# Performance work log

Hardware: AMD Instinct MI355X
Metric: run time of the kernel (lower is better)

Reference implementation:

```python
import jax, jax.numpy as jnp
import numpy as np

B, S, D, H = 2, 2048, 1024, 16
HD = D // H
EPS = 1e-5


def setup_inputs() -> dict:
    key = jax.random.key(0)
    ks = jax.random.split(key, 10)
    s = 1.0 / np.sqrt(D)
    return {
        "x": jax.random.normal(ks[0], (B, S, D), jnp.float32),
        "wq": jax.random.normal(ks[1], (D, D), jnp.float32) * s,
        "bq": jnp.zeros((D,), jnp.float32),
        "wk": jax.random.normal(ks[2], (D, D), jnp.float32) * s,
        "bk": jnp.zeros((D,), jnp.float32),
        "wv": jax.random.normal(ks[3], (D, D), jnp.float32) * s,
        "bv": jnp.zeros((D,), jnp.float32),
        "wo": jax.random.normal(ks[4], (D, D), jnp.float32) * s,
        "bo": jnp.zeros((D,), jnp.float32),
        "gamma": jnp.ones((D,), jnp.float32),
        "beta": jnp.zeros((D,), jnp.float32),
    }


def reference(x, wq, bq, wk, bk, wv, bv, wo, bo, gamma, beta):
    b, s, d = x.shape
    # QKV projections (torch Linear: y = x @ W^T + b)
    q = (x @ wq.T + bq).reshape(b, s, H, HD)
    k = (x @ wk.T + bk).reshape(b, s, H, HD)
    v = (x @ wv.T + bv).reshape(b, s, H, HD)
    # scores: [b, h, s, s], scaled by sqrt(d_model) as in the source
    scores = jnp.einsum("bqhd,bkhd->bhqk", q, k) / np.sqrt(D)
    attn = jax.nn.softmax(scores, axis=-1)
    ctx = jnp.einsum("bhqk,bkhd->bqhd", attn, v).reshape(b, s, d)
    # output projection (dropout is identity in eval mode)
    residual = ctx @ wo.T + bo
    y = x + residual
    # LayerNorm over last dim
    mu = jnp.mean(y, axis=-1, keepdims=True)
    var = jnp.var(y, axis=-1, keepdims=True)
    return (y - mu) / jnp.sqrt(var + EPS) * gamma + beta
```

## Files before the change

### kernel.cpp

```cpp
#include <hip/hip_runtime.h>
#include <math.h>

#define BBATCH 2
#define SS 2048
#define DMODEL 1024
#define NH 16
#define HD 64
#define MM 4096
#define LNEPS 1e-5f
#define CEXP 0.045084220029831766f

typedef __bf16 bf16_t;
typedef __bf16 bf16x4 __attribute__((ext_vector_type(4)));
typedef __bf16 bf16x8 __attribute__((ext_vector_type(8)));
typedef float f32x4 __attribute__((ext_vector_type(4)));

#define MFMA(a, b, c) __builtin_amdgcn_mfma_f32_16x16x32_bf16(a, b, c, 0, 0, 0)

__device__ __forceinline__ void load_lds16(const bf16_t* g, bf16_t* l) {
    __builtin_amdgcn_global_load_lds(
        (const __attribute__((address_space(1))) void*)g,
        (__attribute__((address_space(3))) void*)l, 16, 0, 0);
}

__global__ __launch_bounds__(256) void cvt_kernel(const float* __restrict__ in,
                                                  bf16_t* __restrict__ out) {
    const int i = (blockIdx.x * 256 + threadIdx.x) * 4;
    float4 f = *(const float4*)(in + i);
    bf16x4 o = {(bf16_t)f.x, (bf16_t)f.y, (bf16_t)f.z, (bf16_t)f.w};
    *(bf16x4*)(out + i) = o;
}

__global__ __launch_bounds__(256, 2) void gemm_qkv(
    const bf16_t* __restrict__ A,
    const bf16_t* __restrict__ Wq, const bf16_t* __restrict__ Wk,
    const bf16_t* __restrict__ Wv,
    const float* __restrict__ bq, const float* __restrict__ bk,
    const float* __restrict__ bv,
    bf16_t* __restrict__ qo, bf16_t* __restrict__ ko, bf16_t* __restrict__ vo)
{
    __shared__ bf16_t As[128 * 32];
    __shared__ bf16_t Bs[128 * 32];
    const int tid = threadIdx.x, L = tid & 63, w = tid >> 6;
    const int quad = L >> 4, l15 = L & 15;
    const int wm = (w >> 1) * 64, wn = (w & 1) * 64;
    const int m0 = blockIdx.x * 128;
    const int mat = blockIdx.y >> 3;
    const int n0 = (blockIdx.y & 7) * 128;
    const bf16_t* W = (mat == 0) ? Wq : ((mat == 1) ? Wk : Wv);

    f32x4 acc[4][4] = {};
    for (int k0 = 0; k0 < DMODEL; k0 += 32) {
        __syncthreads();
        #pragma unroll
        for (int i = 0; i < 2; ++i) {
            const int r = w * 32 + i * 16;
            load_lds16(A + (size_t)(m0 + r + (L >> 2)) * DMODEL + k0 + (L & 3) * 8, &As[r * 32]);
            load_lds16(W + (size_t)(n0 + r + (L >> 2)) * DMODEL + k0 + (L & 3) * 8, &Bs[r * 32]);
        }
        __syncthreads();
        bf16x8 af[4], bfr[4];
        #pragma unroll
        for (int t = 0; t < 4; ++t) af[t] = *(const bf16x8*)&As[(wm + t * 16 + l15) * 32 + quad * 8];
        #pragma unroll
        for (int t = 0; t < 4; ++t) bfr[t] = *(const bf16x8*)&Bs[(wn + t * 16 + l15) * 32 + quad * 8];
        #pragma unroll
        for (int mt = 0; mt < 4; ++mt)
            #pragma unroll
            for (int nt = 0; nt < 4; ++nt)
                acc[mt][nt] = MFMA(af[mt], bfr[nt], acc[mt][nt]);
    }

    if (mat < 2) {
        bf16_t* out = (mat == 0) ? qo : ko;
        const float* bias = (mat == 0) ? bq : bk;
        const float sc = (mat == 0) ? CEXP : 1.0f;
        #pragma unroll
        for (int nt = 0; nt < 4; ++nt) {
            const int gn = n0 + wn + nt * 16 + l15;
            const int h = gn >> 6, hd = gn & 63;
            const float bb = bias[gn];
            #pragma unroll
            for (int mt = 0; mt < 4; ++mt)
                #pragma unroll
                for (int r = 0; r < 4; ++r) {
                    const int gm = m0 + wm + mt * 16 + quad * 4 + r;
                    const int b = gm >> 11, s = gm & 2047;
                    out[((size_t)((b * NH + h) * SS + s)) * HD + hd] =
                        (bf16_t)((acc[mt][nt][r] + bb) * sc);
                }
        }
    } else {
        #pragma unroll
        for (int nt = 0; nt < 4; ++nt) {
            const int gn = n0 + wn + nt * 16 + l15;
            const int h = gn >> 6, hd = gn & 63;
            const float bb = bv[gn];
            #pragma unroll
            for (int mt = 0; mt < 4; ++mt) {
                const int gm0 = m0 + wm + mt * 16 + quad * 4;
                const int b = gm0 >> 11, s0 = gm0 & 2047;
                bf16x4 o = {(bf16_t)(acc[mt][nt][0] + bb), (bf16_t)(acc[mt][nt][1] + bb),
                            (bf16_t)(acc[mt][nt][2] + bb), (bf16_t)(acc[mt][nt][3] + bb)};
                *(bf16x4*)(vo + ((size_t)((b * NH + h) * HD + hd)) * SS + s0) = o;
            }
        }
    }
}

__global__ __launch_bounds__(256, 2) void gemm_out(
    const bf16_t* __restrict__ A, const bf16_t* __restrict__ W,
    const float* __restrict__ bias, const float* __restrict__ resid,
    float* __restrict__ out)
{
    __shared__ bf16_t As[128 * 32];
    __shared__ bf16_t Bs[128 * 32];
    const int tid = threadIdx.x, L = tid & 63, w = tid >> 6;
    const int quad = L >> 4, l15 = L & 15;
    const int wm = (w >> 1) * 64, wn = (w & 1) * 64;
    const int m0 = blockIdx.x * 128;
    const int n0 = blockIdx.y * 128;

    f32x4 acc[4][4] = {};
    for (int k0 = 0; k0 < DMODEL; k0 += 32) {
        __syncthreads();
        #pragma unroll
        for (int i = 0; i < 2; ++i) {
            const int r = w * 32 + i * 16;
            load_lds16(A + (size_t)(m0 + r + (L >> 2)) * DMODEL + k0 + (L & 3) * 8, &As[r * 32]);
            load_lds16(W + (size_t)(n0 + r + (L >> 2)) * DMODEL + k0 + (L & 3) * 8, &Bs[r * 32]);
        }
        __syncthreads();
        bf16x8 af[4], bfr[4];
        #pragma unroll
        for (int t = 0; t < 4; ++t) af[t] = *(const bf16x8*)&As[(wm + t * 16 + l15) * 32 + quad * 8];
        #pragma unroll
        for (int t = 0; t < 4; ++t) bfr[t] = *(const bf16x8*)&Bs[(wn + t * 16 + l15) * 32 + quad * 8];
        #pragma unroll
        for (int mt = 0; mt < 4; ++mt)
            #pragma unroll
            for (int nt = 0; nt < 4; ++nt)
                acc[mt][nt] = MFMA(af[mt], bfr[nt], acc[mt][nt]);
    }
    #pragma unroll
    for (int nt = 0; nt < 4; ++nt) {
        const int gn = n0 + wn + nt * 16 + l15;
        const float bb = bias[gn];
        #pragma unroll
        for (int mt = 0; mt < 4; ++mt)
            #pragma unroll
            for (int r = 0; r < 4; ++r) {
                const int gm = m0 + wm + mt * 16 + quad * 4 + r;
                const size_t idx = (size_t)gm * DMODEL + gn;
                out[idx] = acc[mt][nt][r] + bb + resid[idx];
            }
    }
}

__global__ __launch_bounds__(256, 2) void flash_kernel(
    const bf16_t* __restrict__ Q, const bf16_t* __restrict__ K,
    const bf16_t* __restrict__ VT, bf16_t* __restrict__ ctx)
{
    __shared__ bf16_t Kt[64 * 64];
    __shared__ bf16_t Vt[64 * 64];
    const int tid = threadIdx.x, L = tid & 63, w = tid >> 6;
    const int quad = L >> 4, l15 = L & 15, l7 = L & 7;
    const int bh = blockIdx.y, b = bh >> 4, h = bh & 15;
    const int q0 = blockIdx.x * 128;
    const bf16_t* Qb = Q + (size_t)bh * SS * HD;
    const bf16_t* Kb = K + (size_t)bh * SS * HD;
    const bf16_t* Vb = VT + (size_t)bh * HD * SS;

    bf16x8 qf[2][2];
    #pragma unroll
    for (int g = 0; g < 2; ++g) {
        const int qrow = q0 + (w * 2 + g) * 16 + l15;
        #pragma unroll
        for (int c = 0; c < 2; ++c)
            qf[g][c] = *(const bf16x8*)(Qb + (size_t)qrow * HD + c * 32 + quad * 8);
    }

    f32x4 accO[2][4] = {};
    float l_s[2] = {0.f, 0.f};

    const int srow = L >> 3;
    const int schk = ((l7 ^ srow)) * 8;

    for (int kt = 0; kt < SS / 64; ++kt) {
        __syncthreads();
        #pragma unroll
        for (int i = 0; i < 2; ++i) {
            const int r0 = w * 16 + i * 8;
            load_lds16(Kb + (size_t)(kt * 64 + r0 + srow) * HD + schk, &Kt[r0 * 64]);
            load_lds16(Vb + (size_t)(r0 + srow) * SS + kt * 64 + schk, &Vt[r0 * 64]);
        }
        __syncthreads();

        bf16x8 kf[4][2];
        #pragma unroll
        for (int jt = 0; jt < 4; ++jt)
            #pragma unroll
            for (int c = 0; c < 2; ++c)
                kf[jt][c] = *(const bf16x8*)&Kt[(jt * 16 + l15) * 64 + ((c * 4 + quad) ^ l7) * 8];

        bf16x8 vf[4][2];
        #pragma unroll
        for (int mt = 0; mt < 4; ++mt)
            #pragma unroll
            for (int c = 0; c < 2; ++c) {
                const int base = (mt * 16 + l15) * 64;
                const int ch0 = c * 4 + (quad >> 1);
                bf16x4 lo = *(const bf16x4*)&Vt[base + ((ch0 ^ l7) * 8) + (quad & 1) * 4];
                bf16x4 hi = *(const bf16x4*)&Vt[base + (((ch0 + 2) ^ l7) * 8) + (quad & 1) * 4];
                vf[mt][c] = __builtin_shufflevector(lo, hi, 0, 1, 2, 3, 4, 5, 6, 7);
            }

        #pragma unroll
        for (int g = 0; g < 2; ++g) {
            f32x4 st[4];
            #pragma unroll
            for (int jt = 0; jt < 4; ++jt) {
                f32x4 z = {0.f, 0.f, 0.f, 0.f};
                z = MFMA(kf[jt][0], qf[g][0], z);
                z = MFMA(kf[jt][1], qf[g][1], z);
                st[jt] = z;
            }
            #pragma unroll
            for (int jt = 0; jt < 4; ++jt)
                #pragma unroll
                for (int r = 0; r < 4; ++r)
                    st[jt][r] = exp2f(st[jt][r]);
            float s01 = (st[0][0] + st[0][1]) + (st[0][2] + st[0][3]);
            float s23 = (st[1][0] + st[1][1]) + (st[1][2] + st[1][3]);
            float s45 = (st[2][0] + st[2][1]) + (st[2][2] + st[2][3]);
            float s67 = (st[3][0] + st[3][1]) + (st[3][2] + st[3][3]);
            l_s[g] += (s01 + s23) + (s45 + s67);

            bf16x8 pf0, pf1;
            pf0[0] = (bf16_t)st[0][0]; pf0[1] = (bf16_t)st[0][1];
            pf0[2] = (bf16_t)st[0][2]; pf0[3] = (bf16_t)st[0][3];
            pf0[4] = (bf16_t)st[1][0]; pf0[5] = (bf16_t)st[1][1];
            pf0[6] = (bf16_t)st[1][2]; pf0[7] = (bf16_t)st[1][3];
            pf1[0] = (bf16_t)st[2][0]; pf1[1] = (bf16_t)st[2][1];
            pf1[2] = (bf16_t)st[2][2]; pf1[3] = (bf16_t)st[2][3];
            pf1[4] = (bf16_t)st[3][0]; pf1[5] = (bf16_t)st[3][1];
            pf1[6] = (bf16_t)st[3][2]; pf1[7] = (bf16_t)st[3][3];

            #pragma unroll
            for (int mt = 0; mt < 4; ++mt) {
                accO[g][mt] = MFMA(vf[mt][0], pf0, accO[g][mt]);
                accO[g][mt] = MFMA(vf[mt][1], pf1, accO[g][mt]);
            }
        }
    }

    #pragma unroll
    for (int g = 0; g < 2; ++g) {
        float lsum = l_s[g];
        lsum += __shfl_xor(lsum, 16);
        lsum += __shfl_xor(lsum, 32);
        const float inv = 1.0f / lsum;
        const int s = q0 + (w * 2 + g) * 16 + l15;
        #pragma unroll
        for (int mt = 0; mt < 4; ++mt) {
            bf16x4 o = {(bf16_t)(accO[g][mt][0] * inv), (bf16_t)(accO[g][mt][1] * inv),
                        (bf16_t)(accO[g][mt][2] * inv), (bf16_t)(accO[g][mt][3] * inv)};
            *(bf16x4*)(ctx + ((size_t)(b * SS + s)) * DMODEL + h * HD + mt * 16 + quad * 4) = o;
        }
    }
}

__global__ __launch_bounds__(256) void layernorm_kernel(
    float* __restrict__ y, const float* __restrict__ gamma,
    const float* __restrict__ beta)
{
    const int row = blockIdx.x;
    const int tid = threadIdx.x;
    float* yr = y + (size_t)row * DMODEL;
    float4 v = ((const float4*)yr)[tid];
    float s = v.x + v.y + v.z + v.w;
    float ss = v.x * v.x + v.y * v.y + v.z * v.z + v.w * v.w;
    #pragma unroll
    for (int off = 32; off >= 1; off >>= 1) {
        s += __shfl_xor(s, off);
        ss += __shfl_xor(ss, off);
    }
    __shared__ float red[8];
    const int wid = tid >> 6, lane = tid & 63;
    if (lane == 0) { red[wid] = s; red[4 + wid] = ss; }
    __syncthreads();
    s = red[0] + red[1] + red[2] + red[3];
    ss = red[4] + red[5] + red[6] + red[7];
    const float mu = s * (1.0f / DMODEL);
    const float var = ss * (1.0f / DMODEL) - mu * mu;
    const float inv = rsqrtf(var + LNEPS);
    float4 g = ((const float4*)gamma)[tid];
    float4 be = ((const float4*)beta)[tid];
    float4 o;
    o.x = (v.x - mu) * inv * g.x + be.x;
    o.y = (v.y - mu) * inv * g.y + be.y;
    o.z = (v.z - mu) * inv * g.z + be.z;
    o.w = (v.w - mu) * inv * g.w + be.w;
    ((float4*)yr)[tid] = o;
}

extern "C" void kernel_launch(void* const* d_in, const int* in_sizes, int n_in,
                              void* d_out, int out_size, void* d_ws, size_t ws_size,
                              hipStream_t stream)
{
    const float* x     = (const float*)d_in[0];
    const float* wq    = (const float*)d_in[1];
    const float* bq    = (const float*)d_in[2];
    const float* wk    = (const float*)d_in[3];
    const float* bk    = (const float*)d_in[4];
    const float* wv    = (const float*)d_in[5];
    const float* bv    = (const float*)d_in[6];
    const float* wo    = (const float*)d_in[7];
    const float* bo    = (const float*)d_in[8];
    const float* gamma = (const float*)d_in[9];
    const float* beta  = (const float*)d_in[10];
    float* out = (float*)d_out;

    bf16_t* xb  = (bf16_t*)d_ws;
    bf16_t* wqb = xb  + (size_t)4194304;
    bf16_t* wkb = wqb + (size_t)1048576;
    bf16_t* wvb = wkb + (size_t)1048576;
    bf16_t* wob = wvb + (size_t)1048576;
    bf16_t* qb  = wob + (size_t)1048576;
    bf16_t* kb  = qb  + (size_t)4194304;
    bf16_t* vtb = kb  + (size_t)4194304;
    bf16_t* ctx = vtb + (size_t)4194304;

    cvt_kernel<<<4096, 256, 0, stream>>>(x, xb);
    cvt_kernel<<<1024, 256, 0, stream>>>(wq, wqb);
    cvt_kernel<<<1024, 256, 0, stream>>>(wk, wkb);
    cvt_kernel<<<1024, 256, 0, stream>>>(wv, wvb);
    cvt_kernel<<<1024, 256, 0, stream>>>(wo, wob);

    gemm_qkv<<<dim3(32, 24), 256, 0, stream>>>(xb, wqb, wkb, wvb, bq, bk, bv, qb, kb, vtb);
    flash_kernel<<<dim3(16, 32), 256, 0, stream>>>(qb, kb, vtb, ctx);
    gemm_out<<<dim3(32, 8), 256, 0, stream>>>(ctx, wob, bo, x, out);
    layernorm_kernel<<<MM, 256, 0, stream>>>(out, gamma, beta);
}
```

Before: 226.9 us.

## Split flash attention over two key halves with combine kernel, fuse conversions

Splits the attention kernel's key dimension into two halves via a third grid dimension. Each half writes unnormalized bf16 partial outputs and row sums, and a new combine kernel merges and normalizes them. This doubles the number of blocks to fill more CUs. It also enlarges the K/V LDS tiles to 128 keys with a new swizzle, switches to the hardware exp2 builtin with manual bf16 packing, and merges the five conversion launches into one kernel. The cost is an extra kernel plus partial-output memory traffic, and a small precision loss from storing unnormalized partials in bf16.

Result: slower. 311.0 us (+37.0%).

```diff
diff --git a/kernel.cpp b/kernel.cpp
--- a/kernel.cpp
+++ b/kernel.cpp
@@ -1,7 +1,6 @@
 #include <hip/hip_runtime.h>
 #include <math.h>
 
-#define BBATCH 2
 #define SS 2048
 #define DMODEL 1024
 #define NH 16
@@ -14,6 +13,8 @@
 typedef __bf16 bf16x4 __attribute__((ext_vector_type(4)));
 typedef __bf16 bf16x8 __attribute__((ext_vector_type(8)));
 typedef float f32x4 __attribute__((ext_vector_type(4)));
+typedef unsigned int u32;
+typedef u32 u32x4 __attribute__((ext_vector_type(4)));
 
 #define MFMA(a, b, c) __builtin_amdgcn_mfma_f32_16x16x32_bf16(a, b, c, 0, 0, 0)
 
@@ -23,12 +24,37 @@
         (__attribute__((address_space(3))) void*)l, 16, 0, 0);
 }
 
-__global__ __launch_bounds__(256) void cvt_kernel(const float* __restrict__ in,
-                                                  bf16_t* __restrict__ out) {
-    const int i = (blockIdx.x * 256 + threadIdx.x) * 4;
+__device__ __forceinline__ float fast_exp2(float x) {
+#if __has_builtin(__builtin_amdgcn_exp2f)
+    return __builtin_amdgcn_exp2f(x);
+#else
+    return exp2f(x);
+#endif
+}
+
+__device__ __forceinline__ u32 pk2(float lo, float hi) {
+    u32 a = __float_as_uint(lo) + 0x8000u;
+    u32 b = __float_as_uint(hi) + 0x8000u;
+    return (a >> 16) | (b & 0xFFFF0000u);
+}
+
+__global__ __launch_bounds__(256) void cvt_all(
+    const float* __restrict__ x, const float* __restrict__ wq,
+    const float* __restrict__ wk, const float* __restrict__ wv,
+    const float* __restrict__ wo, bf16_t* __restrict__ out)
+{
+    int blk = blockIdx.x;
+    const float* in;
+    size_t off;
+    if (blk < 4096)      { in = x;  off = 0; }
+    else if (blk < 5120) { in = wq; off = 4194304; blk -= 4096; }
+    else if (blk < 6144) { in = wk; off = 5242880; blk -= 5120; }
+    else if (blk < 7168) { in = wv; off = 6291456; blk -= 6144; }
+    else                 { in = wo; off = 7340032; blk -= 7168; }
+    const int i = blk * 1024 + threadIdx.x * 4;
     float4 f = *(const float4*)(in + i);
     bf16x4 o = {(bf16_t)f.x, (bf16_t)f.y, (bf16_t)f.z, (bf16_t)f.w};
-    *(bf16x4*)(out + i) = o;
+    *(bf16x4*)(out + off + i) = o;
 }
 
 __global__ __launch_bounds__(256, 2) void gemm_qkv(
@@ -157,16 +183,18 @@
     }
 }
 
-__global__ __launch_bounds__(256, 2) void flash_kernel(
+__global__ __launch_bounds__(256, 4) void flash_kernel(
     const bf16_t* __restrict__ Q, const bf16_t* __restrict__ K,
-    const bf16_t* __restrict__ VT, bf16_t* __restrict__ ctx)
-{
-    __shared__ bf16_t Kt[64 * 64];
-    __shared__ bf16_t Vt[64 * 64];
+    const bf16_t* __restrict__ VT, bf16_t* __restrict__ Opart,
+    float* __restrict__ lpart)
+{
+    __shared__ bf16_t Kt[128 * 64];
+    __shared__ bf16_t Vt[64 * 128];
     const int tid = threadIdx.x, L = tid & 63, w = tid >> 6;
     const int quad = L >> 4, l15 = L & 15, l7 = L & 7;
     const int bh = blockIdx.y, b = bh >> 4, h = bh & 15;
     const int q0 = blockIdx.x * 128;
+    const int ks = blockIdx.z;
     const bf16_t* Qb = Q + (size_t)bh * SS * HD;
     const bf16_t* Kb = K + (size_t)bh * SS * HD;
     const bf16_t* Vb = VT + (size_t)bh * HD * SS;
@@ -176,98 +204,109 @@
     for (int g = 0; g < 2; ++g) {
         const int qrow = q0 + (w * 2 + g) * 16 + l15;
         #pragma unroll
-        for (int c = 0; c < 2; ++c)
-            qf[g][c] = *(const bf16x8*)(Qb + (size_t)qrow * HD + c * 32 + quad * 8);
+        for (int hc = 0; hc < 2; ++hc)
+            qf[g][hc] = *(const bf16x8*)(Qb + (size_t)qrow * HD + hc * 32 + quad * 8);
     }
 
     f32x4 accO[2][4] = {};
     float l_s[2] = {0.f, 0.f};
 
     const int srow = L >> 3;
-    const int schk = ((l7 ^ srow)) * 8;
-
-    for (int kt = 0; kt < SS / 64; ++kt) {
-        __syncthreads();
-        #pragma unroll
-        for (int i = 0; i < 2; ++i) {
-            const int r0 = w * 16 + i * 8;
-            load_lds16(Kb + (size_t)(kt * 64 + r0 + srow) * HD + schk, &Kt[r0 * 64]);
-            load_lds16(Vb + (size_t)(r0 + srow) * SS + kt * 64 + schk, &Vt[r0 * 64]);
-        }
-        __syncthreads();
-
-        bf16x8 kf[4][2];
-        #pragma unroll
-        for (int jt = 0; jt < 4; ++jt)
-            #pragma unroll
-            for (int c = 0; c < 2; ++c)
-                kf[jt][c] = *(const bf16x8*)&Kt[(jt * 16 + l15) * 64 + ((c * 4 + quad) ^ l7) * 8];
-
-        bf16x8 vf[4][2];
-        #pragma unroll
-        for (int mt = 0; mt < 4; ++mt)
-            #pragma unroll
-            for (int c = 0; c < 2; ++c) {
-                const int base = (mt * 16 + l15) * 64;
+    const int kchk = (l7 ^ srow) * 8;
+    const int vsub = L >> 4;
+
+    for (int kt = 0; kt < 8; ++kt) {
+        const int kb = ks * 1024 + kt * 128;
+        __syncthreads();
+        #pragma unroll
+        for (int i = 0; i < 4; ++i) {
+            const int r0 = w * 32 + i * 8;
+            load_lds16(Kb + (size_t)(kb + r0 + srow) * HD + kchk, &Kt[r0 * 64]);
+        }
+        #pragma unroll
+        for (int i = 0; i < 4; ++i) {
+            const int r0 = w * 16 + i * 4;
+            const int vr = r0 + vsub;
+            load_lds16(Vb + (size_t)vr * SS + kb + ((l15 ^ (vr & 15)) * 8), &Vt[r0 * 128]);
+        }
+        __syncthreads();
+
+        #pragma unroll
+        for (int c = 0; c < 4; ++c) {
+            bf16x8 kf[2][2];
+            #pragma unroll
+            for (int t = 0; t < 2; ++t)
+                #pragma unroll
+                for (int hc = 0; hc < 2; ++hc)
+                    kf[t][hc] = *(const bf16x8*)&Kt[(c * 32 + t * 16 + l15) * 64 +
+                                                    (((hc * 4 + quad) ^ l7) * 8)];
+            bf16x8 vf[4];
+            #pragma unroll
+            for (int mt = 0; mt < 4; ++mt) {
+                const int base = (mt * 16 + l15) * 128;
                 const int ch0 = c * 4 + (quad >> 1);
-                bf16x4 lo = *(const bf16x4*)&Vt[base + ((ch0 ^ l7) * 8) + (quad & 1) * 4];
-                bf16x4 hi = *(const bf16x4*)&Vt[base + (((ch0 + 2) ^ l7) * 8) + (quad & 1) * 4];
-                vf[mt][c] = __builtin_shufflevector(lo, hi, 0, 1, 2, 3, 4, 5, 6, 7);
+                bf16x4 lo = *(const bf16x4*)&Vt[base + ((ch0 ^ l15) * 8) + (quad & 1) * 4];
+                bf16x4 hi = *(const bf16x4*)&Vt[base + (((ch0 + 2) ^ l15) * 8) + (quad & 1) * 4];
+                vf[mt] = __builtin_shufflevector(lo, hi, 0, 1, 2, 3, 4, 5, 6, 7);
             }
 
-        #pragma unroll
-        for (int g = 0; g < 2; ++g) {
-            f32x4 st[4];
-            #pragma unroll
-            for (int jt = 0; jt < 4; ++jt) {
-                f32x4 z = {0.f, 0.f, 0.f, 0.f};
-                z = MFMA(kf[jt][0], qf[g][0], z);
-                z = MFMA(kf[jt][1], qf[g][1], z);
-                st[jt] = z;
+            #pragma unroll
+            for (int g = 0; g < 2; ++g) {
+                f32x4 s0 = {0.f, 0.f, 0.f, 0.f}, s1 = {0.f, 0.f, 0.f, 0.f};
+                s0 = MFMA(kf[0][0], qf[g][0], s0);
+                s0 = MFMA(kf[0][1], qf[g][1], s0);
+                s1 = MFMA(kf[1][0], qf[g][0], s1);
+                s1 = MFMA(kf[1][1], qf[g][1], s1);
+                float p0 = fast_exp2(s0[0]), p1 = fast_exp2(s0[1]);
+                float p2 = fast_exp2(s0[2]), p3 = fast_exp2(s0[3]);
+                float p4 = fast_exp2(s1[0]), p5 = fast_exp2(s1[1]);
+                float p6 = fast_exp2(s1[2]), p7 = fast_exp2(s1[3]);
+                l_s[g] += ((p0 + p1) + (p2 + p3)) + ((p4 + p5) + (p6 + p7));
+                u32x4 pu = {pk2(p0, p1), pk2(p2, p3), pk2(p4, p5), pk2(p6, p7)};
+                bf16x8 pf = __builtin_bit_cast(bf16x8, pu);
+                #pragma unroll
+                for (int mt = 0; mt < 4; ++mt)
+                    accO[g][mt] = MFMA(vf[mt], pf, accO[g][mt]);
             }
-            #pragma unroll
-            for (int jt = 0; jt < 4; ++jt)
-                #pragma unroll
-                for (int r = 0; r < 4; ++r)
-                    st[jt][r] = exp2f(st[jt][r]);
-            float s01 = (st[0][0] + st[0][1]) + (st[0][2] + st[0][3]);
-            float s23 = (st[1][0] + st[1][1]) + (st[1][2] + st[1][3]);
-            float s45 = (st[2][0] + st[2][1]) + (st[2][2] + st[2][3]);
-            float s67 = (st[3][0] + st[3][1]) + (st[3][2] + st[3][3]);
-            l_s[g] += (s01 + s23) + (s45 + s67);
-
-            bf16x8 pf0, pf1;
-            pf0[0] = (bf16_t)st[0][0]; pf0[1] = (bf16_t)st[0][1];
-            pf0[2] = (bf16_t)st[0][2]; pf0[3] = (bf16_t)st[0][3];
-            pf0[4] = (bf16_t)st[1][0]; pf0[5] = (bf16_t)st[1][1];
-            pf0[6] = (bf16_t)st[1][2]; pf0[7] = (bf16_t)st[1][3];
-            pf1[0] = (bf16_t)st[2][0]; pf1[1] = (bf16_t)st[2][1];
-            pf1[2] = (bf16_t)st[2][2]; pf1[3] = (bf16_t)st[2][3];
-            pf1[4] = (bf16_t)st[3][0]; pf1[5] = (bf16_t)st[3][1];
-            pf1[6] = (bf16_t)st[3][2]; pf1[7] = (bf16_t)st[3][3];
-
-            #pragma unroll
-            for (int mt = 0; mt < 4; ++mt) {
-                accO[g][mt] = MFMA(vf[mt][0], pf0, accO[g][mt]);
-                accO[g][mt] = MFMA(vf[mt][1], pf1, accO[g][mt]);
-            }
         }
     }
 
     #pragma unroll
     for (int g = 0; g < 2; ++g) {
-        float lsum = l_s[g];
-        lsum += __shfl_xor(lsum, 16);
-        lsum += __shfl_xor(lsum, 32);
-        const float inv = 1.0f / lsum;
+        float ls = l_s[g];
+        ls += __shfl_xor(ls, 16);
+        ls += __shfl_xor(ls, 32);
         const int s = q0 + (w * 2 + g) * 16 + l15;
+        if (quad == 0) lpart[ks * 65536 + bh * SS + s] = ls;
+        bf16_t* Ob = Opart + (size_t)ks * MM * DMODEL +
+                     ((size_t)(b * SS + s)) * DMODEL + h * HD;
         #pragma unroll
         for (int mt = 0; mt < 4; ++mt) {
-            bf16x4 o = {(bf16_t)(accO[g][mt][0] * inv), (bf16_t)(accO[g][mt][1] * inv),
-                        (bf16_t)(accO[g][mt][2] * inv), (bf16_t)(accO[g][mt][3] * inv)};
-            *(bf16x4*)(ctx + ((size_t)(b * SS + s)) * DMODEL + h * HD + mt * 16 + quad * 4) = o;
-        }
-    }
+            bf16x4 o = {(bf16_t)accO[g][mt][0], (bf16_t)accO[g][mt][1],
+                        (bf16_t)accO[g][mt][2], (bf16_t)accO[g][mt][3]};
+            *(bf16x4*)(Ob + mt * 16 + quad * 4) = o;
+        }
+    }
+}
+
+__global__ __launch_bounds__(256) void combine_kernel(
+    const bf16_t* __restrict__ Opart, const float* __restrict__ lpart,
+    bf16_t* __restrict__ ctx)
+{
+    const int row = blockIdx.x;
+    const int tid = threadIdx.x;
+    const int d = tid * 4;
+    const int b = row >> 11, s = row & 2047, h = d >> 6;
+    const int li = (b * NH + h) * SS + s;
+    const float inv = 1.0f / (lpart[li] + lpart[65536 + li]);
+    const size_t i0 = (size_t)row * DMODEL + d;
+    bf16x4 o0 = *(const bf16x4*)(Opart + i0);
+    bf16x4 o1 = *(const bf16x4*)(Opart + (size_t)MM * DMODEL + i0);
+    bf16x4 o;
+    #pragma unroll
+    for (int k = 0; k < 4; ++k)
+        o[k] = (bf16_t)(((float)o0[k] + (float)o1[k]) * inv);
+    *(bf16x4*)(ctx + i0) = o;
 }
 
 __global__ __launch_bounds__(256) void layernorm_kernel(
@@ -321,24 +360,22 @@
     const float* beta  = (const float*)d_in[10];
     float* out = (float*)d_out;
 
-    bf16_t* xb  = (bf16_t*)d_ws;
-    bf16_t* wqb = xb  + (size_t)4194304;
-    bf16_t* wkb = wqb + (size_t)1048576;
-    bf16_t* wvb = wkb + (size_t)1048576;
-    bf16_t* wob = wvb + (size_t)1048576;
-    bf16_t* qb  = wob + (size_t)1048576;
-    bf16_t* kb  = qb  + (size_t)4194304;
-    bf16_t* vtb = kb  + (size_t)4194304;
-    bf16_t* ctx = vtb + (size_t)4194304;
-
-    cvt_kernel<<<4096, 256, 0, stream>>>(x, xb);
-    cvt_kernel<<<1024, 256, 0, stream>>>(wq, wqb);
-    cvt_kernel<<<1024, 256, 0, stream>>>(wk, wkb);
-    cvt_kernel<<<1024, 256, 0, stream>>>(wv, wvb);
-    cvt_kernel<<<1024, 256, 0, stream>>>(wo, wob);
-
+    bf16_t* xb    = (bf16_t*)d_ws;
+    bf16_t* wqb   = xb + (size_t)4194304;
+    bf16_t* wkb   = wqb + (size_t)1048576;
+    bf16_t* wvb   = wkb + (size_t)1048576;
+    bf16_t* wob   = wvb + (size_t)1048576;
+    bf16_t* qb    = xb + (size_t)8388608;
+    bf16_t* kb    = qb + (size_t)4194304;
+    bf16_t* vtb   = kb + (size_t)4194304;
+    bf16_t* Opart = vtb + (size_t)4194304;
+    float*  lpart = (float*)(xb + (size_t)29360128);
+    bf16_t* ctx   = qb;
+
+    cvt_all<<<8192, 256, 0, stream>>>(x, wq, wk, wv, wo, xb);
     gemm_qkv<<<dim3(32, 24), 256, 0, stream>>>(xb, wqb, wkb, wvb, bq, bk, bv, qb, kb, vtb);
-    flash_kernel<<<dim3(16, 32), 256, 0, stream>>>(qb, kb, vtb, ctx);
+    flash_kernel<<<dim3(16, 32, 2), 256, 0, stream>>>(qb, kb, vtb, Opart, lpart);
+    combine_kernel<<<MM, 256, 0, stream>>>(Opart, lpart, ctx);
     gemm_out<<<dim3(32, 8), 256, 0, stream>>>(ctx, wob, bo, x, out);
     layernorm_kernel<<<MM, 256, 0, stream>>>(out, gamma, beta);
 }
```
